# Optimization experiments

Hardware: AMD Instinct MI355X
Metric: run time of the kernel (lower is better)

## Reference

```python
import jax, jax.numpy as jnp
import numpy as np

N = 262144
IN_DIM = 1024
HID = 256
E = 16
TOP_K = 2


def setup_inputs() -> dict:
    key = jax.random.key(0)
    k1, k2, k3, k4, k5 = jax.random.split(key, 5)
    x = jax.random.normal(k1, (N, IN_DIM), dtype=jnp.float32)
    # Kaiming-ish init scaled for stability
    W1 = jax.random.normal(k2, (IN_DIM, HID), dtype=jnp.float32) * (1.0 / np.sqrt(IN_DIM))
    b1 = jnp.zeros((HID,), dtype=jnp.float32)
    W2 = jax.random.normal(k3, (HID, E), dtype=jnp.float32) * (1.0 / np.sqrt(HID))
    b2 = jnp.zeros((E,), dtype=jnp.float32)
    return {"x": x, "W1": W1, "b1": b1, "W2": W2, "b2": b2}


def reference(x, W1, b1, W2, b2):
    # MLP router: Linear -> ELU -> Linear
    h = jax.nn.elu(x @ W1 + b1)            # [N, HID]
    logits = h @ W2 + b2                   # [N, E]
    # top-k mask: keep top-k logits, set the rest to -inf (scatter semantics)
    vals, idx = jax.lax.top_k(logits, TOP_K)          # [N, K]
    rows = jnp.arange(logits.shape[0])[:, None]        # [N, 1]
    masked = jnp.full_like(logits, -jnp.inf).at[rows, idx].set(vals)
    alpha = jax.nn.softmax(masked, axis=-1)            # [N, E]
    return alpha, logits
```

## Files before the change

### kernel.cpp

```cpp
#include <hip/hip_runtime.h>
#include <math.h>

#define KDIM 1024
#define HID 256
#define NE 16
#define ROWS_BLK 128
#define KCH 32
#define NCHUNK 32
#define CH_BYTES 32768
#define W2T_PLANE (NE * HID)
#define AB_STRIDE 16384
#define BBASE 32768
#define BB_STRIDE 32768
#define SMEM_BYTES 98304

typedef __attribute__((ext_vector_type(8))) _Float16 f16x8;
typedef __attribute__((ext_vector_type(16))) float f32x16;
typedef __attribute__((ext_vector_type(4))) float f32x4;

__device__ __forceinline__ void gld16(const void* g, void* s) {
  __builtin_amdgcn_global_load_lds(
      (const __attribute__((address_space(1))) void*)g,
      (__attribute__((address_space(3))) void*)s, 16, 0, 0);
}

__global__ void prep_w1(const float* __restrict__ W1, _Float16* __restrict__ img) {
  int idx = blockIdx.x * 256 + threadIdx.x;
  int col = idx & 255, kgl = idx >> 8;
  int c = kgl >> 2, kg = kgl & 3, k8 = kgl * 8;
  f16x8 p1, p2;
#pragma unroll
  for (int i = 0; i < 8; ++i) {
    float v = W1[(size_t)(k8 + i) * HID + col];
    _Float16 a = (_Float16)v;
    _Float16 b = (_Float16)((v - (float)a) * 4096.0f);
    p1[i] = a; p2[i] = b;
  }
  size_t off = (size_t)c * 16384 + (size_t)kg * 2048 + (size_t)col * 8;
  *(f16x8*)(img + off) = p1;
  *(f16x8*)(img + off + 8192) = p2;
}

__global__ void prep_w2(const float* __restrict__ W2, _Float16* __restrict__ w2t) {
  int idx = blockIdx.x * 256 + threadIdx.x;
  int e = idx & 15, k = idx >> 4;
  float v = W2[(size_t)k * NE + e];
  _Float16 a = (_Float16)v;
  _Float16 b = (_Float16)((v - (float)a) * 4096.0f);
  w2t[(size_t)e * HID + k] = a;
  w2t[W2T_PLANE + (size_t)e * HID + k] = b;
}

__global__ __launch_bounds__(512, 2) void fused_router(
    const float* __restrict__ x, const _Float16* __restrict__ w1img,
    const _Float16* __restrict__ w2t, const float* __restrict__ bias1,
    const float* __restrict__ bias2, float* __restrict__ outA,
    float* __restrict__ outL)
{
  extern __shared__ char smem[];
  const int t = threadIdx.x, l = t & 63, w = t >> 6;
  const int rowg = w >> 2, colg = w & 3;
  const int l31 = l & 31, hi = l >> 5;
  const int R0 = blockIdx.x * ROWS_BLK;
  const int arow0 = rowg * 64 + l31;
  const int bcol0 = colg * 64 + l31;

  const int xr = t >> 2, xq = t & 3;
  const float* xbase = x + (size_t)(R0 + xr) * KDIM + xq * 8;

  const char* ibase = (const char*)w1img + t * 16;

  f32x16 acc0[2][2], accA[2][2];
#pragma unroll
  for (int rt = 0; rt < 2; ++rt)
#pragma unroll
    for (int ct = 0; ct < 2; ++ct)
#pragma unroll
      for (int j = 0; j < 16; ++j) { acc0[rt][ct][j] = 0.f; accA[rt][ct][j] = 0.f; }

  float xv[8];

#define XLOAD(C_) do {                                                        \
    *(float4*)(xv)     = *(const float4*)(xbase + (size_t)(C_) * KCH);       \
    *(float4*)(xv + 4) = *(const float4*)(xbase + (size_t)(C_) * KCH + 4);   \
  } while (0)

#define BSTAGE(C_, BS_) do {                                                  \
    const char* is_ = ibase + (size_t)(C_) * CH_BYTES;                        \
    char* bd_ = smem + BBASE + (BS_) * BB_STRIDE + t * 16;                    \
    gld16(is_,         bd_);                                                  \
    gld16(is_ + 8192,  bd_ + 8192);                                           \
    gld16(is_ + 16384, bd_ + 16384);                                          \
    gld16(is_ + 24576, bd_ + 24576);                                          \
  } while (0)

#define ASPLIT(BS_) do {                                                      \
    f16x8 pa_, pb_;                                                           \
    _Pragma("unroll") for (int j_ = 0; j_ < 8; ++j_) {                        \
      float v_ = xv[j_];                                                      \
      _Float16 a_ = (_Float16)v_;                                             \
      _Float16 b_ = (_Float16)((v_ - (float)a_) * 4096.0f);                   \
      pa_[j_] = a_; pb_[j_] = b_;                                             \
    }                                                                         \
    int ao_ = (BS_) * AB_STRIDE + xq * 2048 + xr * 16;                        \
    *(f16x8*)(smem + ao_) = pa_;                                              \
    *(f16x8*)(smem + ao_ + 8192) = pb_;                                       \
  } while (0)

#define COMPUTE(BS_) do {                                                     \
    _Pragma("unroll") for (int s_ = 0; s_ < 2; ++s_) {                        \
      const int gg_ = 2 * s_ + hi;                                            \
      f16x8 a1_[2], a2_[2];                                                   \
      _Pragma("unroll") for (int rt_ = 0; rt_ < 2; ++rt_) {                   \
        int ao_ = (BS_) * AB_STRIDE + gg_ * 2048 + (arow0 + 32 * rt_) * 16;   \
        a1_[rt_] = *(const f16x8*)(smem + ao_);                               \
        a2_[rt_] = *(const f16x8*)(smem + ao_ + 8192);                        \
      }                                                                       \
      _Pragma("unroll") for (int ct_ = 0; ct_ < 2; ++ct_) {                   \
        int bo_ = BBASE + (BS_) * BB_STRIDE + gg_ * 4096                      \
                  + (bcol0 + 32 * ct_) * 16;                                  \
        f16x8 b1_ = *(const f16x8*)(smem + bo_);                              \
        f16x8 b2_ = *(const f16x8*)(smem + bo_ + 16384);                      \
        _Pragma("unroll") for (int rt_ = 0; rt_ < 2; ++rt_) {                 \
          acc0[rt_][ct_] = __builtin_amdgcn_mfma_f32_32x32x16_f16(            \
              a1_[rt_], b1_, acc0[rt_][ct_], 0, 0, 0);                        \
          accA[rt_][ct_] = __builtin_amdgcn_mfma_f32_32x32x16_f16(            \
              a1_[rt_], b2_, accA[rt_][ct_], 0, 0, 0);                        \
          accA[rt_][ct_] = __builtin_amdgcn_mfma_f32_32x32x16_f16(            \
              a2_[rt_], b1_, accA[rt_][ct_], 0, 0, 0);                        \
        }                                                                     \
      }                                                                       \
    }                                                                         \
  } while (0)

  XLOAD(0);
  BSTAGE(0, 0);
  ASPLIT(0);
  XLOAD(1);
  __syncthreads();

  int bsel = 0;
#pragma unroll 1
  for (int c = 0; c < NCHUNK; ++c) {
    if (c + 1 < NCHUNK) {
      BSTAGE(c + 1, bsel ^ 1);
      ASPLIT(bsel ^ 1);
      if (c + 2 < NCHUNK) XLOAD(c + 2);
    }
    COMPUTE(bsel);
    __syncthreads();
    bsel ^= 1;
  }

  const float c12 = 1.0f / 4096.0f;
  const int tok = l & 15, g2 = l >> 4;

#pragma unroll 1
  for (int p = 0; p < 2; ++p) {
    __syncthreads();
    if (rowg == p) {
#pragma unroll
      for (int ct = 0; ct < 2; ++ct) {
        int col = bcol0 + 32 * ct;
        float bc = bias1[col];
        int cg = col >> 3, cb = (col & 7) * 2;
#pragma unroll
        for (int rt = 0; rt < 2; ++rt) {
#pragma unroll
          for (int r = 0; r < 16; ++r) {
            int tloc = 32 * rt + (r & 3) + 8 * (r >> 2) + 4 * hi;
            float v = acc0[rt][ct][r] + c12 * accA[rt][ct][r] + bc;
            v = v > 0.f ? v : expm1f(v);
            _Float16 h1 = (_Float16)v;
            _Float16 h2 = (_Float16)((v - (float)h1) * 4096.0f);
            int off = tloc * 512 + ((cg ^ (tloc & 7)) << 4) + cb;
            *(_Float16*)(smem + off) = h1;
            *(_Float16*)(smem + 32768 + off) = h2;
          }
        }
      }
    }
    __syncthreads();
    if (w < 4) {
      int tloc = w * 16 + tok;
      f32x4 L0, LA;
#pragma unroll
      for (int j = 0; j < 4; ++j) { L0[j] = 0.f; LA[j] = 0.f; }
      const _Float16* w2a = w2t + (size_t)tok * HID;
      const _Float16* w2b = w2a + W2T_PLANE;
#pragma unroll
      for (int kt = 0; kt < 8; ++kt) {
        int gg = (kt * 4 + g2) ^ (tloc & 7);
        f16x8 hb1 = *(const f16x8*)(smem + tloc * 512 + (gg << 4));
        f16x8 hb2 = *(const f16x8*)(smem + 32768 + tloc * 512 + (gg << 4));
        f16x8 wa = *(const f16x8*)(w2a + kt * 32 + 8 * g2);
        f16x8 wb = *(const f16x8*)(w2b + kt * 32 + 8 * g2);
        L0 = __builtin_amdgcn_mfma_f32_16x16x32_f16(wa, hb1, L0, 0, 0, 0);
        LA = __builtin_amdgcn_mfma_f32_16x16x32_f16(wa, hb2, LA, 0, 0, 0);
        LA = __builtin_amdgcn_mfma_f32_16x16x32_f16(wb, hb1, LA, 0, 0, 0);
      }
      float4 b2v = *(const float4*)(bias2 + 4 * g2);
      float L[4];
      L[0] = L0[0] + c12 * LA[0] + b2v.x;
      L[1] = L0[1] + c12 * LA[1] + b2v.y;
      L[2] = L0[2] + c12 * LA[2] + b2v.z;
      L[3] = L0[3] + c12 * LA[3] + b2v.w;

      float o1[4], o2[4], o3[4];
#pragma unroll
      for (int j = 0; j < 4; ++j) o1[j] = __shfl_xor(L[j], 16);
#pragma unroll
      for (int j = 0; j < 4; ++j) o2[j] = __shfl_xor(L[j], 32);
#pragma unroll
      for (int j = 0; j < 4; ++j) o3[j] = __shfl_xor(o1[j], 32);

      float all16[16];
#pragma unroll
      for (int cq = 0; cq < 4; ++cq) {
        int xg = cq ^ g2;
#pragma unroll
        for (int j = 0; j < 4; ++j) {
          float v = L[j];
          v = (xg == 1) ? o1[j] : v;
          v = (xg == 2) ? o2[j] : v;
          v = (xg == 3) ? o3[j] : v;
          all16[cq * 4 + j] = v;
        }
      }

      int i1 = 0; float m1 = all16[0];
#pragma unroll
      for (int e = 1; e < 16; ++e) { if (all16[e] > m1) { m1 = all16[e]; i1 = e; } }
      int i2 = -1; float m2 = -INFINITY;
#pragma unroll
      for (int e = 0; e < 16; ++e) { if (e != i1 && all16[e] > m2) { m2 = all16[e]; i2 = e; } }
      float ex = expf(m2 - m1);
      float sden = 1.f + ex;
      float A1 = 1.f / sden;
      float A2 = ex / sden;

      int e0 = 4 * g2;
      float4 alv;
      alv.x = (e0 + 0 == i1) ? A1 : ((e0 + 0 == i2) ? A2 : 0.f);
      alv.y = (e0 + 1 == i1) ? A1 : ((e0 + 1 == i2) ? A2 : 0.f);
      alv.z = (e0 + 2 == i1) ? A1 : ((e0 + 2 == i2) ? A2 : 0.f);
      alv.w = (e0 + 3 == i1) ? A1 : ((e0 + 3 == i2) ? A2 : 0.f);

      size_t orow = (size_t)(R0 + p * 64 + tloc);
      float4 lgv; lgv.x = L[0]; lgv.y = L[1]; lgv.z = L[2]; lgv.w = L[3];
      *(float4*)(outL + orow * NE + e0) = lgv;
      *(float4*)(outA + orow * NE + e0) = alv;
    }
  }
#undef XLOAD
#undef BSTAGE
#undef ASPLIT
#undef COMPUTE
}

extern "C" void kernel_launch(void* const* d_in, const int* in_sizes, int n_in,
                              void* d_out, int out_size, void* d_ws, size_t ws_size,
                              hipStream_t stream) {
  const float* x  = (const float*)d_in[0];
  const float* W1 = (const float*)d_in[1];
  const float* b1 = (const float*)d_in[2];
  const float* W2 = (const float*)d_in[3];
  const float* b2 = (const float*)d_in[4];
  _Float16* w1img = (_Float16*)d_ws;
  _Float16* w2t = w1img + (size_t)NCHUNK * (CH_BYTES / 2);
  float* outA = (float*)d_out;
  const size_t n_tok = (size_t)in_sizes[0] / KDIM;
  float* outL = outA + n_tok * NE;

  prep_w1<<<dim3(128), dim3(256), 0, stream>>>(W1, w1img);
  prep_w2<<<dim3(16), dim3(256), 0, stream>>>(W2, w2t);

  hipFuncSetAttribute((const void*)fused_router,
                      hipFuncAttributeMaxDynamicSharedMemorySize, SMEM_BYTES);
  fused_router<<<dim3((unsigned)(n_tok / ROWS_BLK)), dim3(512), SMEM_BYTES, stream>>>(
      x, w1img, w2t, b1, b2, outA, outL);
}
```

Baseline: 601.1 us.

## Deepen GEMM pipeline to four B buffers with manual vmcnt waits

Result: no change. 602.8 us (+0.3%).

```diff
diff --git a/kernel.cpp b/kernel.cpp
--- a/kernel.cpp
+++ b/kernel.cpp
@@ -9,10 +9,9 @@
 #define NCHUNK 32
 #define CH_BYTES 32768
 #define W2T_PLANE (NE * HID)
-#define AB_STRIDE 16384
-#define BBASE 32768
-#define BB_STRIDE 32768
-#define SMEM_BYTES 98304
+#define ABUF(i) ((i) * 16384)
+#define BBUF(i) (32768 + (i) * 32768)
+#define SMEM_BYTES 163840
 
 typedef __attribute__((ext_vector_type(8))) _Float16 f16x8;
 typedef __attribute__((ext_vector_type(16))) float f32x16;
@@ -78,78 +77,96 @@
 #pragma unroll
       for (int j = 0; j < 16; ++j) { acc0[rt][ct][j] = 0.f; accA[rt][ct][j] = 0.f; }
 
-  float xv[8];
-
-#define XLOAD(C_) do {                                                        \
-    *(float4*)(xv)     = *(const float4*)(xbase + (size_t)(C_) * KCH);       \
-    *(float4*)(xv + 4) = *(const float4*)(xbase + (size_t)(C_) * KCH + 4);   \
-  } while (0)
-
-#define BSTAGE(C_, BS_) do {                                                  \
-    const char* is_ = ibase + (size_t)(C_) * CH_BYTES;                        \
-    char* bd_ = smem + BBASE + (BS_) * BB_STRIDE + t * 16;                    \
-    gld16(is_,         bd_);                                                  \
-    gld16(is_ + 8192,  bd_ + 8192);                                           \
-    gld16(is_ + 16384, bd_ + 16384);                                          \
-    gld16(is_ + 24576, bd_ + 24576);                                          \
-  } while (0)
-
-#define ASPLIT(BS_) do {                                                      \
+  float xvA[8], xvB[8];
+
+#define XLOADV(XV_, C_) do {                                                  \
+    *(float4*)(XV_)     = *(const float4*)(xbase + (size_t)(C_) * KCH);       \
+    *(float4*)((XV_)+4) = *(const float4*)(xbase + (size_t)(C_) * KCH + 4);   \
+  } while (0)
+
+#define BSTAGE_H(C_, BUF_, H_) do {                                           \
+    const char* is_ = ibase + (size_t)(C_) * CH_BYTES + (H_) * 16384;         \
+    char* bd_ = smem + BBUF(BUF_) + (H_) * 16384 + t * 16;                    \
+    gld16(is_,        bd_);                                                   \
+    gld16(is_ + 8192, bd_ + 8192);                                            \
+  } while (0)
+
+#define ASPLITV(XV_, ABW_) do {                                               \
     f16x8 pa_, pb_;                                                           \
     _Pragma("unroll") for (int j_ = 0; j_ < 8; ++j_) {                        \
-      float v_ = xv[j_];                                                      \
+      float v_ = (XV_)[j_];                                                   \
       _Float16 a_ = (_Float16)v_;                                             \
       _Float16 b_ = (_Float16)((v_ - (float)a_) * 4096.0f);                   \
       pa_[j_] = a_; pb_[j_] = b_;                                             \
     }                                                                         \
-    int ao_ = (BS_) * AB_STRIDE + xq * 2048 + xr * 16;                        \
+    int ao_ = ABUF(ABW_) + xq * 2048 + xr * 16;                               \
     *(f16x8*)(smem + ao_) = pa_;                                              \
     *(f16x8*)(smem + ao_ + 8192) = pb_;                                       \
   } while (0)
 
-#define COMPUTE(BS_) do {                                                     \
-    _Pragma("unroll") for (int s_ = 0; s_ < 2; ++s_) {                        \
-      const int gg_ = 2 * s_ + hi;                                            \
-      f16x8 a1_[2], a2_[2];                                                   \
+#define PHASE(S_, ABR_, BBR_) do {                                            \
+    const int gg_ = 2 * (S_) + hi;                                            \
+    f16x8 a1_[2], a2_[2];                                                     \
+    _Pragma("unroll") for (int rt_ = 0; rt_ < 2; ++rt_) {                     \
+      int ao_ = ABUF(ABR_) + gg_ * 2048 + (arow0 + 32 * rt_) * 16;            \
+      a1_[rt_] = *(const f16x8*)(smem + ao_);                                 \
+      a2_[rt_] = *(const f16x8*)(smem + ao_ + 8192);                          \
+    }                                                                         \
+    __builtin_amdgcn_s_setprio(1);                                            \
+    _Pragma("unroll") for (int ct_ = 0; ct_ < 2; ++ct_) {                     \
+      int bo_ = BBUF(BBR_) + gg_ * 4096 + (bcol0 + 32 * ct_) * 16;            \
+      f16x8 b1_ = *(const f16x8*)(smem + bo_);                                \
+      f16x8 b2_ = *(const f16x8*)(smem + bo_ + 16384);                        \
       _Pragma("unroll") for (int rt_ = 0; rt_ < 2; ++rt_) {                   \
-        int ao_ = (BS_) * AB_STRIDE + gg_ * 2048 + (arow0 + 32 * rt_) * 16;   \
-        a1_[rt_] = *(const f16x8*)(smem + ao_);                               \
-        a2_[rt_] = *(const f16x8*)(smem + ao_ + 8192);                        \
-      }                                                                       \
-      _Pragma("unroll") for (int ct_ = 0; ct_ < 2; ++ct_) {                   \
-        int bo_ = BBASE + (BS_) * BB_STRIDE + gg_ * 4096                      \
-                  + (bcol0 + 32 * ct_) * 16;                                  \
-        f16x8 b1_ = *(const f16x8*)(smem + bo_);                              \
-        f16x8 b2_ = *(const f16x8*)(smem + bo_ + 16384);                      \
-        _Pragma("unroll") for (int rt_ = 0; rt_ < 2; ++rt_) {                 \
-          acc0[rt_][ct_] = __builtin_amdgcn_mfma_f32_32x32x16_f16(            \
-              a1_[rt_], b1_, acc0[rt_][ct_], 0, 0, 0);                        \
-          accA[rt_][ct_] = __builtin_amdgcn_mfma_f32_32x32x16_f16(            \
-              a1_[rt_], b2_, accA[rt_][ct_], 0, 0, 0);                        \
-          accA[rt_][ct_] = __builtin_amdgcn_mfma_f32_32x32x16_f16(            \
-              a2_[rt_], b1_, accA[rt_][ct_], 0, 0, 0);                        \
-        }                                                                     \
+        acc0[rt_][ct_] = __builtin_amdgcn_mfma_f32_32x32x16_f16(              \
+            a1_[rt_], b1_, acc0[rt_][ct_], 0, 0, 0);                          \
+        accA[rt_][ct_] = __builtin_amdgcn_mfma_f32_32x32x16_f16(              \
+            a1_[rt_], b2_, accA[rt_][ct_], 0, 0, 0);                          \
+        accA[rt_][ct_] = __builtin_amdgcn_mfma_f32_32x32x16_f16(              \
+            a2_[rt_], b1_, accA[rt_][ct_], 0, 0, 0);                          \
       }                                                                       \
     }                                                                         \
-  } while (0)
-
-  XLOAD(0);
-  BSTAGE(0, 0);
-  ASPLIT(0);
-  XLOAD(1);
-  __syncthreads();
-
-  int bsel = 0;
+    __builtin_amdgcn_s_setprio(0);                                            \
+  } while (0)
+
+#define BODY(C_, ABR_, ABW_, BBR_, BBS_, XV_) do {                            \
+    if ((C_) + 2 < NCHUNK) { BSTAGE_H((C_)+2, BBS_, 0); BSTAGE_H((C_)+2, BBS_, 1); } \
+    if ((C_) + 1 < NCHUNK) ASPLITV(XV_, ABW_);                                \
+    if ((C_) + 3 < NCHUNK) XLOADV(XV_, (C_) + 3);                             \
+    PHASE(0, ABR_, BBR_);                                                     \
+    PHASE(1, ABR_, BBR_);                                                     \
+    __builtin_amdgcn_sched_barrier(0);                                        \
+    if ((C_) <= NCHUNK - 4) {                                                 \
+      asm volatile("s_waitcnt vmcnt(6)" ::: "memory");                        \
+    } else if ((C_) == NCHUNK - 3) {                                          \
+      asm volatile("s_waitcnt vmcnt(4)" ::: "memory");                        \
+    } else {                                                                  \
+      asm volatile("s_waitcnt vmcnt(0)" ::: "memory");                        \
+    }                                                                         \
+    asm volatile("s_waitcnt lgkmcnt(0)" ::: "memory");                        \
+    __builtin_amdgcn_sched_barrier(0);                                        \
+    __builtin_amdgcn_s_barrier();                                             \
+    __builtin_amdgcn_sched_barrier(0);                                        \
+  } while (0)
+
+  XLOADV(xvA, 0);
+  XLOADV(xvB, 1);
+  BSTAGE_H(0, 0, 0); BSTAGE_H(0, 0, 1);
+  BSTAGE_H(1, 1, 0); BSTAGE_H(1, 1, 1);
+  ASPLITV(xvA, 0);
+  XLOADV(xvA, 2);
+  asm volatile("s_waitcnt vmcnt(6)" ::: "memory");
+  asm volatile("s_waitcnt lgkmcnt(0)" ::: "memory");
+  __builtin_amdgcn_sched_barrier(0);
+  __builtin_amdgcn_s_barrier();
+  __builtin_amdgcn_sched_barrier(0);
+
 #pragma unroll 1
-  for (int c = 0; c < NCHUNK; ++c) {
-    if (c + 1 < NCHUNK) {
-      BSTAGE(c + 1, bsel ^ 1);
-      ASPLIT(bsel ^ 1);
-      if (c + 2 < NCHUNK) XLOAD(c + 2);
-    }
-    COMPUTE(bsel);
-    __syncthreads();
-    bsel ^= 1;
+  for (int cb = 0; cb < NCHUNK; cb += 4) {
+    BODY(cb + 0, 0, 1, 0, 2, xvB);
+    BODY(cb + 1, 1, 0, 1, 3, xvA);
+    BODY(cb + 2, 0, 1, 2, 0, xvB);
+    BODY(cb + 3, 1, 0, 3, 1, xvA);
   }
 
   const float c12 = 1.0f / 4096.0f;
@@ -252,10 +269,11 @@
       *(float4*)(outA + orow * NE + e0) = alv;
     }
   }
-#undef XLOAD
-#undef BSTAGE
-#undef ASPLIT
-#undef COMPUTE
+#undef XLOADV
+#undef BSTAGE_H
+#undef ASPLITV
+#undef PHASE
+#undef BODY
 }
 
 extern "C" void kernel_launch(void* const* d_in, const int* in_sizes, int n_in,
```
